# Kernel optimization log

Measured on AMD Instinct MI355X. Metric: run time of the kernel, lower is better.

## Reference

```python
import jax, jax.numpy as jnp
import numpy as np

B, T, F, U = 256, 512, 64, 128

def setup_inputs() -> dict:
    key = jax.random.key(0)
    ks = jax.random.split(key, 8)
    def ortho(k, n):
        a = jax.random.normal(k, (n, n), dtype=jnp.float32)
        q, _ = jnp.linalg.qr(a)
        return q.astype(jnp.float32)
    return {
        "x": jax.random.normal(ks[0], (B, T, F), dtype=jnp.float32),
        "m": jax.random.uniform(ks[1], (B, T, F), dtype=jnp.float32),
        "delta_t": jax.random.uniform(ks[2], (B, T), dtype=jnp.float32),
        "W_z": jax.random.normal(ks[3], (F, U), dtype=jnp.float32) * 0.08,
        "U_z": ortho(ks[4], U),
        "b_z": jnp.zeros((U,), jnp.float32),
        "W_r": jax.random.normal(ks[5], (F, U), dtype=jnp.float32) * 0.08,
        "U_r": ortho(ks[6], U),
        "b_r": jnp.zeros((U,), jnp.float32),
        "W_h": jax.random.normal(ks[7], (F, U), dtype=jnp.float32) * 0.08,
        "U_h": ortho(jax.random.fold_in(key, 99), U),
        "b_h": jnp.zeros((U,), jnp.float32),
        "gamma_x_decay": jnp.ones((F,), jnp.float32),
        "gamma_h_decay": jnp.ones((U,), jnp.float32),
        "mean_imputation": jnp.zeros((F,), jnp.float32),
    }

def reference(x, m, delta_t, W_z, U_z, b_z, W_r, U_r, b_r, W_h, U_h, b_h,
              gamma_x_decay, gamma_h_decay, mean_imputation):
    # delta_t: [B,T] -> [B,T,1]
    dt = delta_t[..., None]
    # input-side decay + imputation (no recurrence -> fully vectorized)
    gamma_x = jnp.exp(-jnp.maximum(0.0, gamma_x_decay) * dt)          # [B,T,F]
    x_dec = m * x + (1.0 - m) * (gamma_x * x + (1.0 - gamma_x) * mean_imputation)
    gamma_h = jnp.exp(-jnp.maximum(0.0, gamma_h_decay) * dt)          # [B,T,U]
    # precompute input projections for all timesteps
    xz = jnp.einsum('btf,fu->btu', x_dec, W_z) + b_z
    xr = jnp.einsum('btf,fu->btu', x_dec, W_r) + b_r
    xh = jnp.einsum('btf,fu->btu', x_dec, W_h) + b_h

    def step(h, inp):
        gz, az, ar, ah = inp            # gamma_h_t [B,U], projected inputs [B,U]
        h_dec = gz * h
        z = jax.nn.sigmoid(az + h_dec @ U_z)
        r = jax.nn.sigmoid(ar + h_dec @ U_r)
        h_hat = jnp.tanh(ah + (r * h_dec) @ U_h)
        h_new = (1.0 - z) * h_dec + z * h_hat
        return h_new, h_new

    h0 = jnp.zeros((x.shape[0], U_z.shape[0]), x.dtype)
    xs = (jnp.swapaxes(gamma_h, 0, 1), jnp.swapaxes(xz, 0, 1),
          jnp.swapaxes(xr, 0, 1), jnp.swapaxes(xh, 0, 1))
    _, hs = jax.lax.scan(step, h0, xs)  # [T,B,U]
    return jnp.swapaxes(hs, 0, 1)       # [B,T,U]
```

## Files before the change

kernel.cpp:

```cpp
#include <hip/hip_runtime.h>

#define B_ 256
#define T_ 512
#define F_ 64
#define U_ 128

typedef _Float16 h2v __attribute__((ext_vector_type(2)));
union U32H2 { unsigned u; h2v h; };

__device__ __forceinline__ float fdot2(unsigned a, unsigned b, float c) {
  U32H2 x, y; x.u = a; y.u = b;
  return __builtin_amdgcn_fdot2(x.h, y.h, c, false);
}
__device__ __forceinline__ unsigned packh2(float a, float b) {
  U32H2 r; r.h[0] = (_Float16)a; r.h[1] = (_Float16)b; return r.u;
}
__device__ __forceinline__ float red4(float v) {
  int t = __builtin_amdgcn_update_dpp(0, __float_as_int(v), 0xB1, 0xF, 0xF, true);
  v += __int_as_float(t);
  t = __builtin_amdgcn_update_dpp(0, __float_as_int(v), 0x4E, 0xF, 0xF, true);
  v += __int_as_float(t);
  return v;
}
__device__ __forceinline__ float fast_sig(float x) {
  return __builtin_amdgcn_rcpf(1.0f + __expf(-x));
}
__device__ __forceinline__ float fast_tanh(float x) {
  return fmaf(-2.0f, __builtin_amdgcn_rcpf(1.0f + __expf(2.0f * x)), 1.0f);
}

#define D4(acc, Hv, Wr, o)                                        \
  acc = fdot2(Hv.x, Wr[(o)], acc);                                \
  acc = fdot2(Hv.y, Wr[(o) + 1], acc);                            \
  acc = fdot2(Hv.z, Wr[(o) + 2], acc);                            \
  acc = fdot2(Hv.w, Wr[(o) + 3], acc);

__global__ __launch_bounds__(256, 1)
__attribute__((amdgpu_waves_per_eu(1, 1)))
void grud_kernel(
    const float* __restrict__ x, const float* __restrict__ m,
    const float* __restrict__ delta_t,
    const float* __restrict__ Wz_, const float* __restrict__ Uz, const float* __restrict__ bz,
    const float* __restrict__ Wr_, const float* __restrict__ Ur, const float* __restrict__ br,
    const float* __restrict__ Wh_, const float* __restrict__ Uh, const float* __restrict__ bh,
    const float* __restrict__ gxd, const float* __restrict__ ghd,
    const float* __restrict__ mi,
    float* __restrict__ out)
{
  const int tid = threadIdx.x;
  const int b   = blockIdx.x;
  const int kg  = tid & 3;
  const int cp  = tid >> 2;
  const int c0  = 2 * cp;
  const bool wr_lane = (kg == 0);

  __shared__ float  s_dt[520];
  __shared__ float  s_ghv[32 * U_];
  __shared__ float  s_hist[32 * U_];
  __shared__ __align__(16) ushort s_x16[32 * F_];
  __shared__ __align__(16) ushort s_hd16[U_];
  __shared__ __align__(16) ushort s_rh16[U_];
  __shared__ float  s_negg[U_];
  __shared__ float  s_gxf[F_];
  __shared__ float  s_mi[F_];

  unsigned uz[32], ur[32], uh[32];
  unsigned wz[16], wr[16], wh[16];
#pragma unroll
  for (int j = 0; j < 16; ++j) {
    const int k0 = 32 * kg + 2 * j;
    uz[j]      = packh2(Uz[k0 * U_ + c0],     Uz[(k0 + 1) * U_ + c0]);
    uz[16 + j] = packh2(Uz[k0 * U_ + c0 + 1], Uz[(k0 + 1) * U_ + c0 + 1]);
    ur[j]      = packh2(Ur[k0 * U_ + c0],     Ur[(k0 + 1) * U_ + c0]);
    ur[16 + j] = packh2(Ur[k0 * U_ + c0 + 1], Ur[(k0 + 1) * U_ + c0 + 1]);
    uh[j]      = packh2(Uh[k0 * U_ + c0],     Uh[(k0 + 1) * U_ + c0]);
    uh[16 + j] = packh2(Uh[k0 * U_ + c0 + 1], Uh[(k0 + 1) * U_ + c0 + 1]);
  }
#pragma unroll
  for (int j = 0; j < 8; ++j) {
    const int f0 = 16 * kg + 2 * j;
    wz[j]     = packh2(Wz_[f0 * U_ + c0],     Wz_[(f0 + 1) * U_ + c0]);
    wz[8 + j] = packh2(Wz_[f0 * U_ + c0 + 1], Wz_[(f0 + 1) * U_ + c0 + 1]);
    wr[j]     = packh2(Wr_[f0 * U_ + c0],     Wr_[(f0 + 1) * U_ + c0]);
    wr[8 + j] = packh2(Wr_[f0 * U_ + c0 + 1], Wr_[(f0 + 1) * U_ + c0 + 1]);
    wh[j]     = packh2(Wh_[f0 * U_ + c0],     Wh_[(f0 + 1) * U_ + c0]);
    wh[8 + j] = packh2(Wh_[f0 * U_ + c0 + 1], Wh_[(f0 + 1) * U_ + c0 + 1]);
  }
  const float bz0 = bz[c0], bz1 = bz[c0 + 1];
  const float br0 = br[c0], br1 = br[c0 + 1];
  const float bh0 = bh[c0], bh1 = bh[c0 + 1];

  {
    const float* dtb = delta_t + (size_t)b * T_;
    s_dt[tid]       = dtb[tid];
    s_dt[tid + 256] = dtb[tid + 256];
    if (tid < 8)   s_dt[512 + tid] = 0.0f;
    if (tid < U_)  { s_negg[tid] = -fmaxf(ghd[tid], 0.0f); ((unsigned*)s_hd16)[tid >> 1] = 0u; }
    if (tid < F_)  { s_gxf[tid] = -fmaxf(gxd[tid], 0.0f); s_mi[tid] = mi[tid]; }
  }
  __syncthreads();

  float hd0 = 0.0f, hd1 = 0.0f;
  float axz0 = 0.f, axz1 = 0.f, axr0 = 0.f, axr1 = 0.f, axh0 = 0.f, axh1 = 0.f;

  for (int t0 = 0; t0 < T_; t0 += 32) {
#pragma unroll
    for (int i = 0; i < 2; ++i) {
      const int e4 = tid + 256 * i;
      const int t = e4 >> 4, f0 = (e4 & 15) << 2;
      const float dtv = s_dt[t0 + t];
      const float4 xv  = *(const float4*)(x + (size_t)(b * T_ + t0 + t) * F_ + f0);
      const float4 mv  = *(const float4*)(m + (size_t)(b * T_ + t0 + t) * F_ + f0);
      const float4 gv  = *(const float4*)(s_gxf + f0);
      const float4 miv = *(const float4*)(s_mi + f0);
      float gx, d0, d1, d2, d3;
      gx = __expf(gv.x * dtv);
      d0 = fmaf(mv.x, xv.x, (1.0f - mv.x) * (gx * xv.x + (1.0f - gx) * miv.x));
      gx = __expf(gv.y * dtv);
      d1 = fmaf(mv.y, xv.y, (1.0f - mv.y) * (gx * xv.y + (1.0f - gx) * miv.y));
      gx = __expf(gv.z * dtv);
      d2 = fmaf(mv.z, xv.z, (1.0f - mv.z) * (gx * xv.z + (1.0f - gx) * miv.z));
      gx = __expf(gv.w * dtv);
      d3 = fmaf(mv.w, xv.w, (1.0f - mv.w) * (gx * xv.w + (1.0f - gx) * miv.w));
      uint2 px; px.x = packh2(d0, d1); px.y = packh2(d2, d3);
      *(uint2*)(s_x16 + 4 * e4) = px;
    }
#pragma unroll
    for (int i = 0; i < 16; ++i) {
      const int e = tid + 256 * i;
      const int t = e >> 7, cc = e & 127;
      s_ghv[e] = __expf(s_negg[cc] * s_dt[t0 + t + 1]);
    }
    __syncthreads();

    {
      const uint4* xp = (const uint4*)(s_x16 + 16 * kg);
      float a0 = 0.f, a1 = 0.f, a2 = 0.f, a3 = 0.f, a4 = 0.f, a5 = 0.f;
#pragma unroll
      for (int q = 0; q < 2; ++q) {
        const uint4 Xv = xp[q];
        D4(a0, Xv, wz, 4 * q)  D4(a1, Xv, wz, 8 + 4 * q)
        D4(a2, Xv, wr, 4 * q)  D4(a3, Xv, wr, 8 + 4 * q)
        D4(a4, Xv, wh, 4 * q)  D4(a5, Xv, wh, 8 + 4 * q)
      }
      axz0 = a0; axz1 = a1; axr0 = a2; axr1 = a3; axh0 = a4; axh1 = a5;
    }

#pragma unroll 1
    for (int tc = 0; tc < 32; ++tc) {
      const uint4* hp = (const uint4*)(s_hd16 + 32 * kg);
      float az0 = axz0, az1 = axz1, ar0 = axr0, ar1 = axr1;
#pragma unroll
      for (int j = 0; j < 4; ++j) {
        const uint4 Hv = hp[j];
        D4(az0, Hv, uz, 4 * j)  D4(az1, Hv, uz, 16 + 4 * j)
        D4(ar0, Hv, ur, 4 * j)  D4(ar1, Hv, ur, 16 + 4 * j)
      }
      const float z0 = fast_sig(red4(az0) + bz0);
      const float z1 = fast_sig(red4(az1) + bz1);
      const float r0 = fast_sig(red4(ar0) + br0);
      const float r1 = fast_sig(red4(ar1) + br1);
      if (wr_lane) ((unsigned*)s_rh16)[cp] = packh2(r0 * hd0, r1 * hd1);
      __syncthreads();

      const float2 ghv = ((const float2*)s_ghv)[tc * 64 + cp];
      const uint4* rp = (const uint4*)(s_rh16 + 32 * kg);
      float ah0 = axh0, ah1 = axh1;
#pragma unroll
      for (int j = 0; j < 4; ++j) {
        const uint4 Rv = rp[j];
        D4(ah0, Rv, uh, 4 * j)  D4(ah1, Rv, uh, 16 + 4 * j)
      }
      if (tc < 31) {
        const uint4* xp = (const uint4*)(s_x16 + (tc + 1) * F_ + 16 * kg);
        float a0 = 0.f, a1 = 0.f, a2 = 0.f, a3 = 0.f, a4 = 0.f, a5 = 0.f;
#pragma unroll
        for (int q = 0; q < 2; ++q) {
          const uint4 Xv = xp[q];
          D4(a0, Xv, wz, 4 * q)  D4(a1, Xv, wz, 8 + 4 * q)
          D4(a2, Xv, wr, 4 * q)  D4(a3, Xv, wr, 8 + 4 * q)
          D4(a4, Xv, wh, 4 * q)  D4(a5, Xv, wh, 8 + 4 * q)
        }
        axz0 = a0; axz1 = a1; axr0 = a2; axr1 = a3; axh0 = a4; axh1 = a5;
      }
      const float hh0 = fast_tanh(red4(ah0) + bh0);
      const float hh1 = fast_tanh(red4(ah1) + bh1);
      const float hn0 = fmaf(z0, hh0 - hd0, hd0);
      const float hn1 = fmaf(z1, hh1 - hd1, hd1);
      hd0 = ghv.x * hn0;
      hd1 = ghv.y * hn1;
      if (wr_lane) {
        ((float2*)s_hist)[tc * 64 + cp] = make_float2(hn0, hn1);
        ((unsigned*)s_hd16)[cp] = packh2(hd0, hd1);
      }
      __syncthreads();
    }

    {
      const float4* h4 = (const float4*)s_hist;
      float4* o4 = (float4*)(out + (size_t)(b * T_ + t0) * U_);
#pragma unroll
      for (int i = 0; i < 4; ++i) o4[tid + 256 * i] = h4[tid + 256 * i];
    }
  }
}

extern "C" void kernel_launch(void* const* d_in, const int* in_sizes, int n_in,
                              void* d_out, int out_size, void* d_ws, size_t ws_size,
                              hipStream_t stream) {
  const float* x   = (const float*)d_in[0];
  const float* m   = (const float*)d_in[1];
  const float* dt  = (const float*)d_in[2];
  const float* Wz  = (const float*)d_in[3];
  const float* Uz  = (const float*)d_in[4];
  const float* bz  = (const float*)d_in[5];
  const float* Wr  = (const float*)d_in[6];
  const float* Ur  = (const float*)d_in[7];
  const float* br  = (const float*)d_in[8];
  const float* Wh  = (const float*)d_in[9];
  const float* Uh  = (const float*)d_in[10];
  const float* bh  = (const float*)d_in[11];
  const float* gxd = (const float*)d_in[12];
  const float* ghd = (const float*)d_in[13];
  const float* mi  = (const float*)d_in[14];

  grud_kernel<<<dim3(B_), dim3(256), 0, stream>>>(
      x, m, dt, Wz, Uz, bz, Wr, Ur, br, Wh, Uh, bh, gxd, ghd, mi, (float*)d_out);
}
```

Baseline: 356.4 us.

## Split GRU-D recurrence K-reduction across 8 lanes with 512-thread blocks

Doubles the threads per block from 256 to 512 so each output pair is reduced over 8 lanes instead of 4. Each lane now holds half as many packed weights and does half the dot-product chain per step, and a third DPP stage (row_shr/half-mirror) finishes the wider reduction. The step body is also reordered: r is computed before z so the r*h write happens sooner, and the next-step input projections are split across the two barrier phases. In exchange each step pays an extra DPP reduction stage and the barriers now cover 8 waves.

After: 456.1 us. +28.0%, slower.

```diff
diff --git a/kernel.cpp b/kernel.cpp
--- a/kernel.cpp
+++ b/kernel.cpp
@@ -15,10 +15,12 @@
 __device__ __forceinline__ unsigned packh2(float a, float b) {
   U32H2 r; r.h[0] = (_Float16)a; r.h[1] = (_Float16)b; return r.u;
 }
-__device__ __forceinline__ float red4(float v) {
+__device__ __forceinline__ float red8(float v) {
   int t = __builtin_amdgcn_update_dpp(0, __float_as_int(v), 0xB1, 0xF, 0xF, true);
   v += __int_as_float(t);
   t = __builtin_amdgcn_update_dpp(0, __float_as_int(v), 0x4E, 0xF, 0xF, true);
+  v += __int_as_float(t);
+  t = __builtin_amdgcn_update_dpp(0, __float_as_int(v), 0x141, 0xF, 0xF, true);
   v += __int_as_float(t);
   return v;
 }
@@ -35,8 +37,8 @@
   acc = fdot2(Hv.z, Wr[(o) + 2], acc);                            \
   acc = fdot2(Hv.w, Wr[(o) + 3], acc);
 
-__global__ __launch_bounds__(256, 1)
-__attribute__((amdgpu_waves_per_eu(1, 1)))
+__global__ __launch_bounds__(512)
+__attribute__((amdgpu_waves_per_eu(2, 2)))
 void grud_kernel(
     const float* __restrict__ x, const float* __restrict__ m,
     const float* __restrict__ delta_t,
@@ -49,8 +51,8 @@
 {
   const int tid = threadIdx.x;
   const int b   = blockIdx.x;
-  const int kg  = tid & 3;
-  const int cp  = tid >> 2;
+  const int kg  = tid & 7;
+  const int cp  = tid >> 3;
   const int c0  = 2 * cp;
   const bool wr_lane = (kg == 0);
 
@@ -64,27 +66,27 @@
   __shared__ float  s_gxf[F_];
   __shared__ float  s_mi[F_];
 
-  unsigned uz[32], ur[32], uh[32];
-  unsigned wz[16], wr[16], wh[16];
-#pragma unroll
-  for (int j = 0; j < 16; ++j) {
-    const int k0 = 32 * kg + 2 * j;
-    uz[j]      = packh2(Uz[k0 * U_ + c0],     Uz[(k0 + 1) * U_ + c0]);
-    uz[16 + j] = packh2(Uz[k0 * U_ + c0 + 1], Uz[(k0 + 1) * U_ + c0 + 1]);
-    ur[j]      = packh2(Ur[k0 * U_ + c0],     Ur[(k0 + 1) * U_ + c0]);
-    ur[16 + j] = packh2(Ur[k0 * U_ + c0 + 1], Ur[(k0 + 1) * U_ + c0 + 1]);
-    uh[j]      = packh2(Uh[k0 * U_ + c0],     Uh[(k0 + 1) * U_ + c0]);
-    uh[16 + j] = packh2(Uh[k0 * U_ + c0 + 1], Uh[(k0 + 1) * U_ + c0 + 1]);
-  }
+  unsigned uz[16], ur[16], uh[16];
+  unsigned wz[8],  wr[8],  wh[8];
 #pragma unroll
   for (int j = 0; j < 8; ++j) {
-    const int f0 = 16 * kg + 2 * j;
+    const int k0 = 16 * kg + 2 * j;
+    uz[j]     = packh2(Uz[k0 * U_ + c0],     Uz[(k0 + 1) * U_ + c0]);
+    uz[8 + j] = packh2(Uz[k0 * U_ + c0 + 1], Uz[(k0 + 1) * U_ + c0 + 1]);
+    ur[j]     = packh2(Ur[k0 * U_ + c0],     Ur[(k0 + 1) * U_ + c0]);
+    ur[8 + j] = packh2(Ur[k0 * U_ + c0 + 1], Ur[(k0 + 1) * U_ + c0 + 1]);
+    uh[j]     = packh2(Uh[k0 * U_ + c0],     Uh[(k0 + 1) * U_ + c0]);
+    uh[8 + j] = packh2(Uh[k0 * U_ + c0 + 1], Uh[(k0 + 1) * U_ + c0 + 1]);
+  }
+#pragma unroll
+  for (int j = 0; j < 4; ++j) {
+    const int f0 = 8 * kg + 2 * j;
     wz[j]     = packh2(Wz_[f0 * U_ + c0],     Wz_[(f0 + 1) * U_ + c0]);
-    wz[8 + j] = packh2(Wz_[f0 * U_ + c0 + 1], Wz_[(f0 + 1) * U_ + c0 + 1]);
+    wz[4 + j] = packh2(Wz_[f0 * U_ + c0 + 1], Wz_[(f0 + 1) * U_ + c0 + 1]);
     wr[j]     = packh2(Wr_[f0 * U_ + c0],     Wr_[(f0 + 1) * U_ + c0]);
-    wr[8 + j] = packh2(Wr_[f0 * U_ + c0 + 1], Wr_[(f0 + 1) * U_ + c0 + 1]);
+    wr[4 + j] = packh2(Wr_[f0 * U_ + c0 + 1], Wr_[(f0 + 1) * U_ + c0 + 1]);
     wh[j]     = packh2(Wh_[f0 * U_ + c0],     Wh_[(f0 + 1) * U_ + c0]);
-    wh[8 + j] = packh2(Wh_[f0 * U_ + c0 + 1], Wh_[(f0 + 1) * U_ + c0 + 1]);
+    wh[4 + j] = packh2(Wh_[f0 * U_ + c0 + 1], Wh_[(f0 + 1) * U_ + c0 + 1]);
   }
   const float bz0 = bz[c0], bz1 = bz[c0 + 1];
   const float br0 = br[c0], br1 = br[c0 + 1];
@@ -92,8 +94,7 @@
 
   {
     const float* dtb = delta_t + (size_t)b * T_;
-    s_dt[tid]       = dtb[tid];
-    s_dt[tid + 256] = dtb[tid + 256];
+    if (tid < 512) s_dt[tid] = dtb[tid];
     if (tid < 8)   s_dt[512 + tid] = 0.0f;
     if (tid < U_)  { s_negg[tid] = -fmaxf(ghd[tid], 0.0f); ((unsigned*)s_hd16)[tid >> 1] = 0u; }
     if (tid < F_)  { s_gxf[tid] = -fmaxf(gxd[tid], 0.0f); s_mi[tid] = mi[tid]; }
@@ -104,9 +105,8 @@
   float axz0 = 0.f, axz1 = 0.f, axr0 = 0.f, axr1 = 0.f, axh0 = 0.f, axh1 = 0.f;
 
   for (int t0 = 0; t0 < T_; t0 += 32) {
-#pragma unroll
-    for (int i = 0; i < 2; ++i) {
-      const int e4 = tid + 256 * i;
+    {
+      const int e4 = tid;
       const int t = e4 >> 4, f0 = (e4 & 15) << 2;
       const float dtv = s_dt[t0 + t];
       const float4 xv  = *(const float4*)(x + (size_t)(b * T_ + t0 + t) * F_ + f0);
@@ -126,73 +126,65 @@
       *(uint2*)(s_x16 + 4 * e4) = px;
     }
 #pragma unroll
-    for (int i = 0; i < 16; ++i) {
-      const int e = tid + 256 * i;
+    for (int i = 0; i < 8; ++i) {
+      const int e = tid + 512 * i;
       const int t = e >> 7, cc = e & 127;
       s_ghv[e] = __expf(s_negg[cc] * s_dt[t0 + t + 1]);
     }
     __syncthreads();
 
     {
-      const uint4* xp = (const uint4*)(s_x16 + 16 * kg);
+      const uint4 Xv = *(const uint4*)(s_x16 + 8 * kg);
       float a0 = 0.f, a1 = 0.f, a2 = 0.f, a3 = 0.f, a4 = 0.f, a5 = 0.f;
-#pragma unroll
-      for (int q = 0; q < 2; ++q) {
-        const uint4 Xv = xp[q];
-        D4(a0, Xv, wz, 4 * q)  D4(a1, Xv, wz, 8 + 4 * q)
-        D4(a2, Xv, wr, 4 * q)  D4(a3, Xv, wr, 8 + 4 * q)
-        D4(a4, Xv, wh, 4 * q)  D4(a5, Xv, wh, 8 + 4 * q)
-      }
+      D4(a0, Xv, wz, 0)  D4(a1, Xv, wz, 4)
+      D4(a2, Xv, wr, 0)  D4(a3, Xv, wr, 4)
+      D4(a4, Xv, wh, 0)  D4(a5, Xv, wh, 4)
       axz0 = a0; axz1 = a1; axr0 = a2; axr1 = a3; axh0 = a4; axh1 = a5;
     }
 
 #pragma unroll 1
     for (int tc = 0; tc < 32; ++tc) {
-      const uint4* hp = (const uint4*)(s_hd16 + 32 * kg);
+      const uint4* hp = (const uint4*)(s_hd16 + 16 * kg);
+      const uint4 H0 = hp[0], H1 = hp[1];
       float az0 = axz0, az1 = axz1, ar0 = axr0, ar1 = axr1;
-#pragma unroll
-      for (int j = 0; j < 4; ++j) {
-        const uint4 Hv = hp[j];
-        D4(az0, Hv, uz, 4 * j)  D4(az1, Hv, uz, 16 + 4 * j)
-        D4(ar0, Hv, ur, 4 * j)  D4(ar1, Hv, ur, 16 + 4 * j)
+      D4(ar0, H0, ur, 0)  D4(ar1, H0, ur, 8)
+      D4(ar0, H1, ur, 4)  D4(ar1, H1, ur, 12)
+      D4(az0, H0, uz, 0)  D4(az1, H0, uz, 8)
+      D4(az0, H1, uz, 4)  D4(az1, H1, uz, 12)
+      const float r0 = fast_sig(red8(ar0) + br0);
+      const float r1 = fast_sig(red8(ar1) + br1);
+      if (wr_lane) ((unsigned*)s_rh16)[cp] = packh2(r0 * hd0, r1 * hd1);
+      const float z0 = fast_sig(red8(az0) + bz0);
+      const float z1 = fast_sig(red8(az1) + bz1);
+      if (tc < 31) {
+        const uint4 Xv = *(const uint4*)(s_x16 + (tc + 1) * F_ + 8 * kg);
+        float a0 = 0.f, a1 = 0.f;
+        D4(a0, Xv, wz, 0)  D4(a1, Xv, wz, 4)
+        axz0 = a0; axz1 = a1;
       }
-      const float z0 = fast_sig(red4(az0) + bz0);
-      const float z1 = fast_sig(red4(az1) + bz1);
-      const float r0 = fast_sig(red4(ar0) + br0);
-      const float r1 = fast_sig(red4(ar1) + br1);
-      if (wr_lane) ((unsigned*)s_rh16)[cp] = packh2(r0 * hd0, r1 * hd1);
       __syncthreads();
 
       const float2 ghv = ((const float2*)s_ghv)[tc * 64 + cp];
-      const uint4* rp = (const uint4*)(s_rh16 + 32 * kg);
+      const uint4* rp = (const uint4*)(s_rh16 + 16 * kg);
+      const uint4 R0 = rp[0], R1 = rp[1];
       float ah0 = axh0, ah1 = axh1;
-#pragma unroll
-      for (int j = 0; j < 4; ++j) {
-        const uint4 Rv = rp[j];
-        D4(ah0, Rv, uh, 4 * j)  D4(ah1, Rv, uh, 16 + 4 * j)
-      }
-      if (tc < 31) {
-        const uint4* xp = (const uint4*)(s_x16 + (tc + 1) * F_ + 16 * kg);
-        float a0 = 0.f, a1 = 0.f, a2 = 0.f, a3 = 0.f, a4 = 0.f, a5 = 0.f;
-#pragma unroll
-        for (int q = 0; q < 2; ++q) {
-          const uint4 Xv = xp[q];
-          D4(a0, Xv, wz, 4 * q)  D4(a1, Xv, wz, 8 + 4 * q)
-          D4(a2, Xv, wr, 4 * q)  D4(a3, Xv, wr, 8 + 4 * q)
-          D4(a4, Xv, wh, 4 * q)  D4(a5, Xv, wh, 8 + 4 * q)
-        }
-        axz0 = a0; axz1 = a1; axr0 = a2; axr1 = a3; axh0 = a4; axh1 = a5;
-      }
-      const float hh0 = fast_tanh(red4(ah0) + bh0);
-      const float hh1 = fast_tanh(red4(ah1) + bh1);
+      D4(ah0, R0, uh, 0)  D4(ah1, R0, uh, 8)
+      D4(ah0, R1, uh, 4)  D4(ah1, R1, uh, 12)
+      const float hh0 = fast_tanh(red8(ah0) + bh0);
+      const float hh1 = fast_tanh(red8(ah1) + bh1);
       const float hn0 = fmaf(z0, hh0 - hd0, hd0);
       const float hn1 = fmaf(z1, hh1 - hd1, hd1);
       hd0 = ghv.x * hn0;
       hd1 = ghv.y * hn1;
-      if (wr_lane) {
-        ((float2*)s_hist)[tc * 64 + cp] = make_float2(hn0, hn1);
-        ((unsigned*)s_hd16)[cp] = packh2(hd0, hd1);
+      if (wr_lane) ((unsigned*)s_hd16)[cp] = packh2(hd0, hd1);
+      if (tc < 31) {
+        const uint4 Xv = *(const uint4*)(s_x16 + (tc + 1) * F_ + 8 * kg);
+        float a2 = 0.f, a3 = 0.f, a4 = 0.f, a5 = 0.f;
+        D4(a2, Xv, wr, 0)  D4(a3, Xv, wr, 4)
+        D4(a4, Xv, wh, 0)  D4(a5, Xv, wh, 4)
+        axr0 = a2; axr1 = a3; axh0 = a4; axh1 = a5;
       }
+      if (wr_lane) ((float2*)s_hist)[tc * 64 + cp] = make_float2(hn0, hn1);
       __syncthreads();
     }
 
@@ -200,7 +192,7 @@
       const float4* h4 = (const float4*)s_hist;
       float4* o4 = (float4*)(out + (size_t)(b * T_ + t0) * U_);
 #pragma unroll
-      for (int i = 0; i < 4; ++i) o4[tid + 256 * i] = h4[tid + 256 * i];
+      for (int i = 0; i < 2; ++i) o4[tid + 512 * i] = h4[tid + 512 * i];
     }
   }
 }
@@ -224,6 +216,6 @@
   const float* ghd = (const float*)d_in[13];
   const float* mi  = (const float*)d_in[14];
 
-  grud_kernel<<<dim3(B_), dim3(256), 0, stream>>>(
+  grud_kernel<<<dim3(B_), dim3(512), 0, stream>>>(
       x, m, dt, Wz, Uz, bz, Wr, Ur, br, Wh, Uh, bh, gxd, ghd, mi, (float*)d_out);
 }
```
